# Performance work log

Measured on AMD Instinct MI355X. Metric: run time of the kernel, lower is better.

## Reference

```python
import jax, jax.numpy as jnp
import numpy as np

B, HIMG, WIMG = 8, 24, 24
WIDTH, NCH, CW = 1024, 8, 128
NHEADS, HD = 8, 16
HALF = HD // 2
NFREQ, VOCAB, NCLS = 32, 256, 10
HIDDEN = 4096
EPS = 1e-6
LAMBDA_INIT = 0.8 - 0.6 * float(np.exp(-0.3 * 0.0))  # layer_idx = 0


def rmsnorm(x, w, eps=EPS):
    return x * jax.lax.rsqrt(jnp.mean(x * x, axis=-1, keepdims=True) + eps) * w


def causal_attn(q, k, v, scale):
    # q,k: [B,H,L,d2], v: [B,H,L,D]
    L = q.shape[2]
    scores = jnp.einsum('bhqd,bhkd->bhqk', q, k) * scale
    mask = jnp.tril(jnp.ones((L, L), dtype=bool))
    scores = jnp.where(mask, scores, -jnp.inf)
    return jnp.einsum('bhqk,bhkd->bhqd', jax.nn.softmax(scores, axis=-1), v)


def diff_attn(h, qkv_w, qkv_b, qn_w, kn_w, hn_w, lq1, lk1, lq2, lk2, ow, ob):
    Bb, L, C = h.shape
    qkv = jax.nn.silu(h @ qkv_w + qkv_b).reshape(Bb, L, 3, NHEADS, HD)
    q, k, v = qkv[:, :, 0], qkv[:, :, 1], qkv[:, :, 2]
    t = lambda a: a.transpose(0, 2, 1, 3)  # [B,L,H,d] -> [B,H,L,d]
    q1 = t(rmsnorm(q[..., :HALF], qn_w)); q2 = t(rmsnorm(q[..., HALF:], qn_w))
    k1 = t(rmsnorm(k[..., :HALF], kn_w)); k2 = t(rmsnorm(k[..., HALF:], kn_w))
    v = t(v)
    lam = jnp.exp(jnp.dot(lq1, lk1)) - jnp.exp(jnp.dot(lq2, lk2)) + LAMBDA_INIT
    scale = 1.0 / np.sqrt(HALF)
    out1 = causal_attn(q1, k1, v, scale)
    out2 = causal_attn(q2, k2, v, scale)
    diff = rmsnorm(out1 - lam * out2, hn_w) * (1.0 - LAMBDA_INIT)
    out = diff.transpose(0, 2, 1, 3).reshape(Bb, L, C)
    return jax.nn.silu(out @ ow + ob)


def setup_inputs() -> dict:
    key = jax.random.key(0)
    ks = iter(jax.random.split(key, 64))
    n = lambda shape, s=0.02: jax.random.normal(next(ks), shape, jnp.float32) * s
    return dict(
        x=jax.random.uniform(next(ks), (B, HIMG, WIMG), jnp.float32),
        top_k=4,
        pixel_embed=n((VOCAB, WIDTH)),
        freq_h=n((NFREQ,), 0.1), freq_w=n((NFREQ,), 0.1),
        phase_h=jnp.zeros((NFREQ,), jnp.float32), phase_w=jnp.zeros((NFREQ,), jnp.float32),
        pos_proj_w=n((4 * NFREQ, WIDTH)), pos_proj_b=jnp.zeros((WIDTH,), jnp.float32),
        embed_norm_w=jnp.ones((WIDTH,), jnp.float32),
        se_w1=n((WIDTH, WIDTH // 4)), se_b1=jnp.zeros((WIDTH // 4,), jnp.float32),
        se_w2=n((WIDTH // 4, WIDTH)), se_b2=jnp.zeros((WIDTH,), jnp.float32),
        mix_norm_w=jnp.ones((WIDTH,), jnp.float32),
        mlp_w1=n((WIDTH, HIDDEN)), mlp_b1=jnp.zeros((HIDDEN,), jnp.float32),
        mlp_w2=n((HIDDEN, WIDTH)), mlp_b2=jnp.zeros((WIDTH,), jnp.float32),
        mlp_norm_w=jnp.ones((WIDTH,), jnp.float32),
        router_w=n((WIDTH, NCH)), router_b=jnp.zeros((NCH,), jnp.float32),
        qkv_w=n((NCH, CW, 3 * CW)), qkv_b=jnp.zeros((NCH, 3 * CW), jnp.float32),
        q_norm_w=jnp.ones((NCH, HALF), jnp.float32), k_norm_w=jnp.ones((NCH, HALF), jnp.float32),
        head_norm_w=jnp.ones((NCH, HD), jnp.float32),
        lam_q1=n((NCH, HALF), 0.1), lam_k1=n((NCH, HALF), 0.1),
        lam_q2=n((NCH, HALF), 0.1), lam_k2=n((NCH, HALF), 0.1),
        out_w=n((NCH, CW, CW)), out_b=jnp.zeros((NCH, CW), jnp.float32),
        seg_norm_w=jnp.ones((NCH, CW), jnp.float32),
        head_w=n((WIDTH, NCLS)), head_b=jnp.zeros((NCLS,), jnp.float32),
    )


def reference(x, top_k, pixel_embed, freq_h, freq_w, phase_h, phase_w, pos_proj_w,
              pos_proj_b, embed_norm_w, se_w1, se_b1, se_w2, se_b2, mix_norm_w,
              mlp_w1, mlp_b1, mlp_w2, mlp_b2, mlp_norm_w, router_w, router_b,
              qkv_w, qkv_b, q_norm_w, k_norm_w, head_norm_w, lam_q1, lam_k1,
              lam_q2, lam_k2, out_w, out_b, seg_norm_w, head_w, head_b):
    Bb, H, W = x.shape
    L = H * W
    # LearnedSinusoidal2DEmbed
    hp = jnp.arange(H, dtype=jnp.float32) / H
    wp = jnp.arange(W, dtype=jnp.float32) / W
    fh = jax.nn.softplus(freq_h) * 10.0
    fw = jax.nn.softplus(freq_w) * 10.0
    ha = hp[:, None] * fh + phase_h          # [H, NFREQ]
    wa = wp[:, None] * fw + phase_w
    h_enc = jnp.concatenate([jnp.sin(ha), jnp.cos(ha)], -1)
    w_enc = jnp.concatenate([jnp.sin(wa), jnp.cos(wa)], -1)
    pos = jnp.concatenate([jnp.broadcast_to(h_enc[:, None], (H, W, 2 * NFREQ)),
                           jnp.broadcast_to(w_enc[None, :], (H, W, 2 * NFREQ))], -1)
    pos = pos @ pos_proj_w + pos_proj_b      # [H, W, WIDTH]
    xi = jnp.clip((x * 255.0).astype(jnp.int32), 0, 255).reshape(Bb, L)
    h = pixel_embed[xi] + pos.reshape(1, L, WIDTH)
    h = rmsnorm(h, embed_norm_w)
    # ChannelMixer: SE + RMSNorm residual, MLP residual, top-k router
    s = jnp.mean(h, axis=1)
    s = jax.nn.sigmoid(jax.nn.silu(s @ se_w1 + se_b1) @ se_w2 + se_b2)
    h = h + rmsnorm(h * s[:, None, :] - h, mix_norm_w)
    h = h + rmsnorm(jax.nn.silu(h @ mlp_w1 + mlp_b1) @ mlp_w2 + mlp_b2, mlp_norm_w)
    logits_r = jnp.mean(h, axis=1) @ router_w + router_b   # [B, NCH]
    tv, ti = jax.lax.top_k(logits_r, top_k)
    rw = jnp.zeros_like(logits_r).at[jnp.arange(Bb)[:, None], ti].set(jax.nn.softmax(tv, axis=-1))
    # ChannelSegment: per-channel differential attention expert, routed
    outs = []
    for i in range(NCH):
        hi = h[..., i * CW:(i + 1) * CW]
        o = diff_attn(hi, qkv_w[i], qkv_b[i], q_norm_w[i], k_norm_w[i], head_norm_w[i],
                      lam_q1[i], lam_k1[i], lam_q2[i], lam_k2[i], out_w[i], out_b[i])
        hi = hi + rmsnorm(o, seg_norm_w[i])
        outs.append(hi * rw[:, i][:, None, None])
    h = jnp.concatenate(outs, axis=-1)
    # classifier head
    return jnp.mean(h, axis=1) @ head_w + head_b
```

## Files before the change

### kernel.cpp

```cpp
#include <hip/hip_runtime.h>
#include <math.h>

typedef __bf16 bf16;
typedef __bf16 bf16x8 __attribute__((ext_vector_type(8)));
typedef __bf16 bf16x4 __attribute__((ext_vector_type(4)));
typedef __bf16 bf16x2 __attribute__((ext_vector_type(2)));
typedef float f32x4 __attribute__((ext_vector_type(4)));
typedef short s16x4 __attribute__((ext_vector_type(4)));

constexpr int Bsz = 8, HIMG = 24, WIMG = 24;
constexpr int Lq = 576;
constexpr int WIDTH = 1024, NCH = 8, CW = 128;
constexpr int NHEADS = 8, HD = 16, HALF = 8;
constexpr float EPS = 1e-6f;
constexpr float LAMINIT = 0.2f;
constexpr float QSCALE_E = 0.35355339059327373f * 1.4426950408889634f;
constexpr int ROWS = Bsz * Lq;

__device__ __forceinline__ float fexp2(float x) {
#if __has_builtin(__builtin_amdgcn_exp2f)
  return __builtin_amdgcn_exp2f(x);
#else
  return exp2f(x);
#endif
}

constexpr size_t B_HB    = 0;
constexpr size_t B_G2B   = B_HB    + 9437184;
constexpr size_t B_ENCB  = B_G2B   + 9437184;
constexpr size_t B_POSWT = B_ENCB  + 163840;
constexpr size_t B_QKVWT = B_POSWT + 262144;
constexpr size_t B_OWT   = B_QKVWT + 786432;
constexpr size_t B_SE    = B_OWT   + 262144;
constexpr size_t B_T1    = B_SE    + 32768;
constexpr size_t B_MP    = B_T1    + 8192;
constexpr size_t B_RW    = B_MP    + 524288;
constexpr size_t B_LAM   = B_RW    + 256;
constexpr size_t B_POOL  = B_LAM   + 256;

__device__ __forceinline__ float blockReduceSum256(float v, float* red) {
  #pragma unroll
  for (int off = 32; off; off >>= 1) v += __shfl_down(v, off, 64);
  int lane = threadIdx.x & 63, wid = threadIdx.x >> 6;
  if (lane == 0) red[wid] = v;
  __syncthreads();
  float total = 0.f;
  #pragma unroll
  for (int i = 0; i < 4; i++) total += red[i];
  return total;
}
__device__ __forceinline__ float silu(float x) { return x / (1.f + __expf(-x)); }

__device__ __forceinline__ void gl16(const bf16* g, bf16* l) {
  __builtin_amdgcn_global_load_lds(
      (const __attribute__((address_space(1))) void*)g,
      (__attribute__((address_space(3))) void*)l, 16, 0, 0);
}

__device__ __forceinline__ f32x4 mfma16(bf16x4 a, bf16x4 b, f32x4 c) {
#if __has_builtin(__builtin_amdgcn_mfma_f32_16x16x16bf16_1k)
  union { bf16x4 h; s16x4 s; } ua, ub;
  ua.h = a; ub.h = b;
  return __builtin_amdgcn_mfma_f32_16x16x16bf16_1k(ua.s, ub.s, c, 0, 0, 0);
#else
  f32x4 d = c;
  asm volatile("v_mfma_f32_16x16x16_bf16 %0, %1, %2, %0"
               : "+v"(d) : "v"(a), "v"(b));
  return d;
#endif
}

__global__ __launch_bounds__(256) void k_tcast(const float* __restrict__ W,
    bf16* __restrict__ Wt, int K, int N) {
  __shared__ float t[32][33];
  int n0 = blockIdx.x * 32, k0 = blockIdx.y * 32;
  long zo = (long)blockIdx.z * K * N;
  int tid = threadIdx.x;
  int r = tid >> 3, c4 = (tid & 7) * 4;
  const float4 v = *(const float4*)(W + zo + (long)(k0 + r) * N + n0 + c4);
  t[c4 + 0][r] = v.x; t[c4 + 1][r] = v.y; t[c4 + 2][r] = v.z; t[c4 + 3][r] = v.w;
  __syncthreads();
  bf16* dst = Wt + zo + (long)(n0 + r) * K + k0 + c4;
  dst[0] = (bf16)t[r][c4 + 0]; dst[1] = (bf16)t[r][c4 + 1];
  dst[2] = (bf16)t[r][c4 + 2]; dst[3] = (bf16)t[r][c4 + 3];
}

__global__ void k_enc_b(const float* __restrict__ fh, const float* __restrict__ fw,
                        const float* __restrict__ ph, const float* __restrict__ pw,
                        bf16* __restrict__ enc) {
  int idx = blockIdx.x * blockDim.x + threadIdx.x;
  if (idx >= Lq * 128) return;
  int l = idx >> 7, c = idx & 127;
  int hh = l / WIMG, ww = l % WIMG;
  float v;
  if (c < 64) {
    int f = c & 31;
    float fr = log1pf(__expf(fh[f])) * 10.f;
    float a = (hh / (float)HIMG) * fr + ph[f];
    v = (c < 32) ? sinf(a) : cosf(a);
  } else {
    int f = c & 31;
    float fr = log1pf(__expf(fw[f])) * 10.f;
    float a = (ww / (float)WIMG) * fr + pw[f];
    v = (c < 96) ? sinf(a) : cosf(a);
  }
  enc[idx] = (bf16)v;
}

template <int ACT, int OUTBF>
__global__ __launch_bounds__(256) void gemm_bt(
    const bf16* __restrict__ A, int lda, long aZs,
    const bf16* __restrict__ Bt, long bZs,
    const float* __restrict__ bias, int biasZs,
    void* __restrict__ Cv, int ldc, long cZs,
    int M, int N, int K) {
  __shared__ bf16 As[128 * 32];
  __shared__ bf16 Bs[128 * 32];
  int tid = threadIdx.x;
  int m0 = blockIdx.y * 128, n0 = blockIdx.x * 128;
  int z = blockIdx.z;
  const bf16* Ab = A + (long)z * aZs;
  const bf16* Bb = Bt + (long)z * bZs;
  f32x4 acc[4][4] = {};
  int wv = tid >> 6, lane = tid & 63;
  int wrow = (wv >> 1) * 64, wcol = (wv & 1) * 64;
  int lm = lane & 15, lq = lane >> 4;
  const bf16* ag = Ab + (long)(m0 + (tid >> 2)) * lda + (tid & 3) * 8;
  const bf16* bg = Bb + (long)(n0 + (tid >> 2)) * K + (tid & 3) * 8;
  bf16* asd = As + tid * 8;
  bf16* bsd = Bs + tid * 8;
  for (int k0 = 0; k0 < K; k0 += 32) {
    gl16(ag + k0, asd);
    gl16(ag + k0 + 64L * lda, asd + 2048);
    gl16(bg + k0, bsd);
    gl16(bg + k0 + 64L * K, bsd + 2048);
    __syncthreads();
    bf16x8 af[4], bfr[4];
    #pragma unroll
    for (int i = 0; i < 4; i++) {
      af[i]  = *(const bf16x8*)(As + (wrow + i * 16 + lm) * 32 + lq * 8);
      bfr[i] = *(const bf16x8*)(Bs + (wcol + i * 16 + lm) * 32 + lq * 8);
    }
    #pragma unroll
    for (int i = 0; i < 4; i++)
      #pragma unroll
      for (int j = 0; j < 4; j++)
        acc[i][j] = __builtin_amdgcn_mfma_f32_16x16x32_bf16(af[i], bfr[j], acc[i][j], 0, 0, 0);
    __syncthreads();
  }
  long cz = (long)z * cZs;
  const float* bz = bias ? bias + (long)z * biasZs : nullptr;
  #pragma unroll
  for (int i = 0; i < 4; i++) {
    int row = m0 + wrow + i * 16 + lq * 4;
    #pragma unroll
    for (int j = 0; j < 4; j++) {
      int col = n0 + wcol + j * 16 + lm;
      float bv = bz ? bz[col] : 0.f;
      #pragma unroll
      for (int r = 0; r < 4; r++) {
        float v = acc[i][j][r] + bv;
        if (ACT == 1) v = silu(v);
        long off = cz + (long)(row + r) * ldc + col;
        if (OUTBF) ((bf16*)Cv)[off] = (bf16)v;
        else       ((float*)Cv)[off] = v;
      }
    }
  }
}

template <int ACT, int OUTBF, int ACC>
__global__ __launch_bounds__(256) void gemm64(
    const bf16* __restrict__ A, int lda, long aZs,
    const bf16* __restrict__ Bt, int ldb, long bZs,
    const float* __restrict__ bias, int biasZs,
    void* __restrict__ Cv, int ldc, long cZs,
    int M, int N, int K) {
  __shared__ bf16 As[64 * 32];
  __shared__ bf16 Bs[128 * 32];
  int tid = threadIdx.x;
  int m0 = blockIdx.y * 64, n0 = blockIdx.x * 128;
  int z = blockIdx.z;
  const bf16* Ab = A + (long)z * aZs;
  const bf16* Bb = Bt + (long)z * bZs;
  f32x4 acc[4][2] = {};
  int wv = tid >> 6, lane = tid & 63;
  int lm = lane & 15, lq = lane >> 4;
  int wcol = wv * 32;
  const bf16* ag = Ab + (long)(m0 + (tid >> 2)) * lda + (tid & 3) * 8;
  const bf16* bg = Bb + (long)(n0 + (tid >> 2)) * ldb + (tid & 3) * 8;
  bf16* asd = As + tid * 8;
  bf16* bsd = Bs + tid * 8;
  for (int k0 = 0; k0 < K; k0 += 32) {
    if (tid < 256) gl16(ag + k0, asd);
    gl16(bg + k0, bsd);
    gl16(bg + k0 + 64L * ldb, bsd + 2048);
    __syncthreads();
    bf16x8 af[4], bfr[2];
    #pragma unroll
    for (int i = 0; i < 4; i++)
      af[i] = *(const bf16x8*)(As + (i * 16 + lm) * 32 + lq * 8);
    #pragma unroll
    for (int j = 0; j < 2; j++)
      bfr[j] = *(const bf16x8*)(Bs + (wcol + j * 16 + lm) * 32 + lq * 8);
    #pragma unroll
    for (int i = 0; i < 4; i++)
      #pragma unroll
      for (int j = 0; j < 2; j++)
        acc[i][j] = __builtin_amdgcn_mfma_f32_16x16x32_bf16(af[i], bfr[j], acc[i][j], 0, 0, 0);
    __syncthreads();
  }
  long cz = (long)z * cZs;
  const float* bz = bias ? bias + (long)z * biasZs : nullptr;
  #pragma unroll
  for (int i = 0; i < 4; i++) {
    int row = m0 + i * 16 + lq * 4;
    #pragma unroll
    for (int j = 0; j < 2; j++) {
      int col = n0 + wcol + j * 16 + lm;
      float bv = bz ? bz[col] : 0.f;
      #pragma unroll
      for (int r = 0; r < 4; r++) {
        float v = acc[i][j][r] + bv;
        long off = cz + (long)(row + r) * ldc + col;
        if (ACC) v += (float)((bf16*)Cv)[off];
        if (ACT == 1) v = silu(v);
        if (OUTBF) ((bf16*)Cv)[off] = (bf16)v;
        else       ((float*)Cv)[off] = v;
      }
    }
  }
}

__global__ __launch_bounds__(256) void k_embed(const float* __restrict__ x,
    const float* __restrict__ emb, const float* __restrict__ pos,
    const float* __restrict__ nw, bf16* __restrict__ h) {
  __shared__ float red[4];
  int row = blockIdx.x;
  int l = row % Lq;
  int xi = (int)(x[row] * 255.f);
  xi = min(max(xi, 0), 255);
  const float* er = emb + (long)xi * WIDTH;
  const float* pr = pos + (long)l * WIDTH;
  int c0 = threadIdx.x * 4;
  float v[4]; float ss = 0.f;
  #pragma unroll
  for (int i = 0; i < 4; i++) { v[i] = er[c0 + i] + pr[c0 + i]; ss += v[i] * v[i]; }
  ss = blockReduceSum256(ss, red);
  float r = rsqrtf(ss / WIDTH + EPS);
  bf16* hr = h + (long)row * WIDTH;
  #pragma unroll
  for (int i = 0; i < 4; i++) hr[c0 + i] = (bf16)(v[i] * r * nw[c0 + i]);
}

__global__ void k_meanl_p(const bf16* __restrict__ h, float* __restrict__ part) {
  int lp = blockIdx.x, b = blockIdx.y, t = threadIdx.x;
  const bf16* p = h + ((long)b * Lq + (long)lp * 36) * WIDTH + t * 4;
  float a0 = 0, a1 = 0, a2 = 0, a3 = 0;
  for (int l = 0; l < 36; l++) {
    bf16x4 v = *(const bf16x4*)(p + (long)l * WIDTH);
    a0 += (float)v[0]; a1 += (float)v[1]; a2 += (float)v[2]; a3 += (float)v[3];
  }
  float* dst = part + ((long)b * 16 + lp) * WIDTH + t * 4;
  dst[0] = a0; dst[1] = a1; dst[2] = a2; dst[3] = a3;
}

__global__ __launch_bounds__(256) void k_se1(const float* __restrict__ part,
    const float* __restrict__ w1, const float* __restrict__ b1,
    float* __restrict__ t1) {
  __shared__ float sv[1024];
  __shared__ float red[256];
  int jb = blockIdx.x, b = blockIdx.y, t = threadIdx.x;
  for (int c = t; c < 1024; c += 256) {
    float a = 0.f;
    #pragma unroll
    for (int lp = 0; lp < 16; lp++) a += part[((long)b * 16 + lp) * 1024 + c];
    sv[c] = a * (1.f / 576.f);
  }
  __syncthreads();
  int j = t & 7, pt = t >> 3;
  int j0 = jb * 8;
  float acc = 0.f;
  int c0 = pt * 32;
  #pragma unroll 8
  for (int c = c0; c < c0 + 32; c++) acc += sv[c] * w1[c * 256 + j0 + j];
  red[t] = acc;
  __syncthreads();
  if (t < 8) {
    float a = b1[j0 + t];
    #pragma unroll
    for (int p = 0; p < 32; p++) a += red[p * 8 + t];
    t1[b * 256 + j0 + t] = silu(a);
  }
}

__global__ __launch_bounds__(256) void k_se2(const float* __restrict__ t1,
    const float* __restrict__ w2, const float* __restrict__ b2,
    float* __restrict__ s) {
  __shared__ float red[256];
  int jb = blockIdx.x, b = blockIdx.y, t = threadIdx.x;
  int j = t & 31, pt = t >> 5;
  int j0 = jb * 32;
  const float* tb = t1 + b * 256;
  float acc = 0.f;
  int c0 = pt * 32;
  #pragma unroll 8
  for (int c = c0; c < c0 + 32; c++) acc += tb[c] * w2[c * 1024 + j0 + j];
  red[t] = acc;
  __syncthreads();
  if (t < 32) {
    float a = b2[j0 + t];
    #pragma unroll
    for (int p = 0; p < 8; p++) a += red[p * 32 + t];
    s[b * 1024 + j0 + t] = 1.f / (1.f + __expf(-a));
  }
}

__global__ __launch_bounds__(256) void k_mix_b(bf16* __restrict__ h,
    const float* __restrict__ s, const float* __restrict__ mw) {
  __shared__ float red[4];
  int row = blockIdx.x;
  int b = row / Lq;
  bf16* hr = h + (long)row * WIDTH;
  const float* sb = s + b * WIDTH;
  int c0 = threadIdx.x * 4;
  float hv[4], y[4]; float ss = 0.f;
  #pragma unroll
  for (int i = 0; i < 4; i++) {
    hv[i] = (float)hr[c0 + i];
    y[i] = hv[i] * (sb[c0 + i] - 1.f); ss += y[i] * y[i];
  }
  ss = blockReduceSum256(ss, red);
  float r = rsqrtf(ss / WIDTH + EPS);
  #pragma unroll
  for (int i = 0; i < 4; i++) hr[c0 + i] = (bf16)(hv[i] + y[i] * r * mw[c0 + i]);
}

__global__ __launch_bounds__(256) void k_addnorm_b(bf16* __restrict__ h,
    const bf16* __restrict__ g, const float* __restrict__ mw) {
  __shared__ float red[4];
  int row = blockIdx.x;
  bf16* hr = h + (long)row * WIDTH;
  const bf16* gr = g + (long)row * WIDTH;
  int c0 = threadIdx.x * 4;
  float y[4]; float ss = 0.f;
  #pragma unroll
  for (int i = 0; i < 4; i++) { y[i] = (float)gr[c0 + i]; ss += y[i] * y[i]; }
  ss = blockReduceSum256(ss, red);
  float r = rsqrtf(ss / WIDTH + EPS);
  #pragma unroll
  for (int i = 0; i < 4; i++)
    hr[c0 + i] = (bf16)((float)hr[c0 + i] + y[i] * r * mw[c0 + i]);
}

__global__ __launch_bounds__(256) void k_router(const float* __restrict__ part,
    const float* __restrict__ rwgt, const float* __restrict__ rb,
    const float* __restrict__ lq1, const float* __restrict__ lk1,
    const float* __restrict__ lq2, const float* __restrict__ lk2,
    float* __restrict__ rw, float* __restrict__ lam) {
  __shared__ float sv[1024];
  __shared__ float red[256];
  __shared__ float lg[8];
  int b = blockIdx.x, t = threadIdx.x;
  for (int c = t; c < 1024; c += 256) {
    float a = 0.f;
    #pragma unroll
    for (int lp = 0; lp < 16; lp++) a += part[((long)b * 16 + lp) * 1024 + c];
    sv[c] = a * (1.f / 576.f);
  }
  __syncthreads();
  int j = t & 7, pt = t >> 3;
  float acc = 0.f;
  int c0 = pt * 32;
  #pragma unroll 8
  for (int c = c0; c < c0 + 32; c++) acc += sv[c] * rwgt[c * 8 + j];
  red[t] = acc;
  __syncthreads();
  if (t < 8) {
    float a = rb[t];
    for (int p = 0; p < 32; p++) a += red[p * 8 + t];
    lg[t] = a;
  }
  __syncthreads();
  if (t == 0) {
    float v[8]; bool sel[8];
    #pragma unroll
    for (int i = 0; i < 8; i++) { v[i] = lg[i]; sel[i] = false; }
    int idxs[4]; float vals[4];
    for (int s = 0; s < 4; s++) {
      int bi = -1; float bv = -1e30f;
      for (int i = 0; i < 8; i++) if (!sel[i] && v[i] > bv) { bv = v[i]; bi = i; }
      sel[bi] = true; idxs[s] = bi; vals[s] = bv;
    }
    float m = vals[0], den = 0.f, e[4];
    for (int s = 0; s < 4; s++) { e[s] = __expf(vals[s] - m); den += e[s]; }
    for (int i = 0; i < 8; i++) rw[b * 8 + i] = 0.f;
    for (int s = 0; s < 4; s++) rw[b * 8 + idxs[s]] = e[s] / den;
  }
  if (b == 0 && t >= 8 && t < 16) {
    int c = t - 8;
    float d1 = 0.f, d2 = 0.f;
    for (int i = 0; i < 8; i++) {
      d1 += lq1[c * 8 + i] * lk1[c * 8 + i];
      d2 += lq2[c * 8 + i] * lk2[c * 8 + i];
    }
    lam[c] = __expf(d1) - __expf(d2) + LAMINIT;
  }
}

__global__ __launch_bounds__(256) void k_attn_mfma(
    const bf16* __restrict__ qkv, const float* __restrict__ lam,
    const float* __restrict__ hnw, const float* __restrict__ qn,
    const float* __restrict__ kn, bf16* __restrict__ dc) {
  __shared__ bf16 Ks[576 * 16];
  __shared__ bf16 Vt[16 * 584];
  int tid = threadIdx.x;
  int slice = blockIdx.x; int zc = slice >> 3, b = slice & 7;
  int head = blockIdx.z;
  const bf16* qkvb = qkv + ((long)zc * ROWS + (long)b * Lq) * 384;
  for (int i = tid; i < 1152; i += 256) {
    int row = i >> 1, hf = i & 1;
    gl16(qkvb + (long)row * 384 + 128 + head * 16 + hf * 8, Ks + i * 8);
  }
  for (int i = tid; i < 1152; i += 256) {
    int row = i >> 1, dh = i & 1;
    bf16x8 v = *(const bf16x8*)(qkvb + (long)row * 384 + 256 + head * 16 + dh * 8);
    #pragma unroll
    for (int j = 0; j < 8; j++) Vt[(dh * 8 + j) * 584 + row] = v[j];
  }
  __syncthreads();
  {
    float kw[8];
    #pragma unroll
    for (int j = 0; j < 8; j++) kw[j] = kn[zc * 8 + j];
    for (int i = tid; i < 1152; i += 256) {
      bf16x8 kv = *(const bf16x8*)(Ks + i * 8);
      float f[8], s = 0.f;
      #pragma unroll
      for (int j = 0; j < 8; j++) { f[j] = (float)kv[j]; s += f[j] * f[j]; }
      float r = rsqrtf(s * 0.125f + EPS);
      bf16x8 o;
      #pragma unroll
      for (int j = 0; j < 8; j++) o[j] = (bf16)(f[j] * r * kw[j]);
      *(bf16x8*)(Ks + i * 8) = o;
    }
  }
  __syncthreads();
  int wv = tid >> 6, lane = tid & 63;
  int lm = lane & 15, lq = lane >> 4;
  float lamv = lam[zc];
  float hwv[4];
  #pragma unroll
  for (int r = 0; r < 4; r++) hwv[r] = hnw[zc * 16 + lq * 4 + r] * (1.f - LAMINIT);
  float qw[8];
  #pragma unroll
  for (int j = 0; j < 8; j++) qw[j] = qn[zc * 8 + j];
  int u = blockIdx.y * 4 + wv;
  int prA, prB, prC;
  if (u < 6) { prA = u + 2; prB = 17 - u; prC = -1; }
  else       { int v2 = u - 6; prA = v2; prB = 8 + v2; prC = 11 - v2; }
  for (int pi = 0; pi < 3; pi++) {
    int pr = (pi == 0) ? prA : (pi == 1) ? prB : prC;
    if (pr < 0) continue;
    bf16x8 bq0[2] = {{}, {}}, bq1[2] = {{}, {}};
    if (lq < 2) {
      #pragma unroll
      for (int tile = 0; tile < 2; tile++) {
        bf16x8 t8 = *(const bf16x8*)(
            qkvb + (long)(pr * 32 + tile * 16 + lm) * 384 + head * 16 + lq * 8);
        float f[8], s = 0.f;
        #pragma unroll
        for (int j = 0; j < 8; j++) { f[j] = (float)t8[j]; s += f[j] * f[j]; }
        float r = rsqrtf(s * 0.125f + EPS) * QSCALE_E;
        bf16x8 n;
        #pragma unroll
        for (int j = 0; j < 8; j++) n[j] = (bf16)(f[j] * r * qw[j]);
        if (lq == 0) bq0[tile] = n; else bq1[tile] = n;
      }
    }
    f32x4 o[2][2] = {};
    float den[2][2] = {};
    for (int kc = 0; kc <= pr; kc++) {
      f32x4 sT[2][2][2] = {};
      #pragma unroll
      for (int t = 0; t < 2; t++) {
        bf16x8 aK = {};
        if (lq < 2) aK = *(const bf16x8*)(Ks + (kc * 32 + t * 16 + lm) * 16 + lq * 8);
        #pragma unroll
        for (int tile = 0; tile < 2; tile++) {
          sT[t][tile][0] = __builtin_amdgcn_mfma_f32_16x16x32_bf16(aK, bq0[tile], sT[t][tile][0], 0, 0, 0);
          sT[t][tile][1] = __builtin_amdgcn_mfma_f32_16x16x32_bf16(aK, bq1[tile], sT[t][tile][1], 0, 0, 0);
        }
      }
      bool diag = (kc == pr);
      #pragma unroll
      for (int t = 0; t < 2; t++) {
        bf16x4 aV = *(const bf16x4*)(Vt + lm * 584 + kc * 32 + t * 16 + lq * 4);
        #pragma unroll
        for (int tile = 0; tile < 2; tile++) {
          if (diag && tile == 0 && t == 1) continue;
          bool masked = diag && (tile == t);
          #pragma unroll
          for (int h2 = 0; h2 < 2; h2++) {
            bf16x4 pb;
            float dsum = 0.f;
            #pragma unroll
            for (int r = 0; r < 4; r++) {
              float ev = fexp2(sT[t][tile][h2][r]);
              if (masked && (lq * 4 + r > lm)) ev = 0.f;
              dsum += ev;
              pb[r] = (bf16)ev;
            }
            den[tile][h2] += dsum;
            o[tile][h2] = mfma16(aV, pb, o[tile][h2]);
          }
        }
      }
    }
    #pragma unroll
    for (int tile = 0; tile < 2; tile++)
      #pragma unroll
      for (int h2 = 0; h2 < 2; h2++) {
        den[tile][h2] += __shfl_xor(den[tile][h2], 16);
        den[tile][h2] += __shfl_xor(den[tile][h2], 32);
      }
    #pragma unroll
    for (int tile = 0; tile < 2; tile++) {
      float inv1 = 1.f / den[tile][0];
      float inv2 = lamv / den[tile][1];
      float dff[4]; float ss = 0.f;
      #pragma unroll
      for (int r = 0; r < 4; r++) {
        dff[r] = o[tile][0][r] * inv1 - o[tile][1][r] * inv2;
        ss += dff[r] * dff[r];
      }
      ss += __shfl_xor(ss, 16);
      ss += __shfl_xor(ss, 32);
      float rr = rsqrtf(ss * 0.0625f + EPS);
      bf16x4 outp;
      #pragma unroll
      for (int r = 0; r < 4; r++) outp[r] = (bf16)(dff[r] * rr * hwv[r]);
      long rowg = (long)zc * ROWS + (long)b * Lq + pr * 32 + tile * 16 + lm;
      *(bf16x4*)(dc + rowg * 128 + head * 16 + lq * 4) = outp;
    }
  }
}

__global__ __launch_bounds__(64) void k_segpool(const bf16* __restrict__ h,
    const bf16* __restrict__ op, const float* __restrict__ segw,
    const float* __restrict__ rw, float* __restrict__ part) {
  int lp = blockIdx.x, b = blockIdx.y, ch = blockIdx.z;
  int t = threadIdx.x;
  int c0 = t * 2;
  float w0 = segw[ch * 128 + c0], w1 = segw[ch * 128 + c0 + 1];
  float rwv = rw[b * 8 + ch];
  float a0 = 0.f, a1 = 0.f;
  for (int l = 0; l < 72; l++) {
    int row = b * Lq + lp * 72 + l;
    const bf16* oprow = op + (long)ch * ROWS * CW + (long)row * CW;
    bf16x2 yv = *(const bf16x2*)(oprow + c0);
    float y0 = (float)yv[0], y1 = (float)yv[1];
    float ss = y0 * y0 + y1 * y1;
    #pragma unroll
    for (int m = 1; m < 64; m <<= 1) ss += __shfl_xor(ss, m);
    float r = rsqrtf(ss * (1.f / 128.f) + EPS);
    bf16x2 hv = *(const bf16x2*)(h + (long)row * WIDTH + ch * 128 + c0);
    a0 += ((float)hv[0] + y0 * r * w0) * rwv;
    a1 += ((float)hv[1] + y1 * r * w1) * rwv;
  }
  float* dst = part + ((long)b * 8 + lp) * 1024 + ch * 128 + c0;
  dst[0] = a0; dst[1] = a1;
}

__global__ __launch_bounds__(256) void k_head(const float* __restrict__ part,
    const float* __restrict__ hw, const float* __restrict__ hb, float* __restrict__ out) {
  __shared__ float pool[1024];
  __shared__ float red[256];
  int b = blockIdx.x, t = threadIdx.x;
  for (int c = t; c < 1024; c += 256) {
    float a = 0.f;
    #pragma unroll
    for (int lp = 0; lp < 8; lp++) a += part[((long)b * 8 + lp) * 1024 + c];
    pool[c] = a * (1.f / 576.f);
  }
  __syncthreads();
  int j = t & 15, pt = t >> 4;
  float acc = 0.f;
  if (j < 10)
    for (int c = pt * 64; c < pt * 64 + 64; c++)
      acc += pool[c] * hw[c * 10 + j];
  red[t] = acc;
  __syncthreads();
  if (t < 10) {
    float a = hb[t];
    for (int p = 0; p < 16; p++) a += red[p * 16 + t];
    out[b * 10 + t] = a;
  }
}

extern "C" void kernel_launch(void* const* d_in, const int* in_sizes, int n_in,
                              void* d_out, int out_size, void* d_ws, size_t ws_size,
                              hipStream_t stream) {
  const float* x          = (const float*)d_in[0];
  const float* pixel_embed= (const float*)d_in[2];
  const float* freq_h     = (const float*)d_in[3];
  const float* freq_w     = (const float*)d_in[4];
  const float* phase_h    = (const float*)d_in[5];
  const float* phase_w    = (const float*)d_in[6];
  const float* pos_proj_w = (const float*)d_in[7];
  const float* pos_proj_b = (const float*)d_in[8];
  const float* embed_norm = (const float*)d_in[9];
  const float* se_w1      = (const float*)d_in[10];
  const float* se_b1      = (const float*)d_in[11];
  const float* se_w2      = (const float*)d_in[12];
  const float* se_b2      = (const float*)d_in[13];
  const float* mix_norm   = (const float*)d_in[14];
  const float* mlp_w1     = (const float*)d_in[15];
  const float* mlp_b1     = (const float*)d_in[16];
  const float* mlp_w2     = (const float*)d_in[17];
  const float* mlp_b2     = (const float*)d_in[18];
  const float* mlp_norm   = (const float*)d_in[19];
  const float* router_w   = (const float*)d_in[20];
  const float* router_b   = (const float*)d_in[21];
  const float* qkv_w      = (const float*)d_in[22];
  const float* qkv_b      = (const float*)d_in[23];
  const float* q_norm_w   = (const float*)d_in[24];
  const float* k_norm_w   = (const float*)d_in[25];
  const float* head_norm_w= (const float*)d_in[26];
  const float* lam_q1     = (const float*)d_in[27];
  const float* lam_k1     = (const float*)d_in[28];
  const float* lam_q2     = (const float*)d_in[29];
  const float* lam_k2     = (const float*)d_in[30];
  const float* out_w      = (const float*)d_in[31];
  const float* out_b      = (const float*)d_in[32];
  const float* seg_norm_w = (const float*)d_in[33];
  const float* head_w     = (const float*)d_in[34];
  const float* head_b     = (const float*)d_in[35];

  char* W = (char*)d_ws;
  bf16*  HB    = (bf16*)(W + B_HB);
  bf16*  G2B   = (bf16*)(W + B_G2B);
  bf16*  ENCB  = (bf16*)(W + B_ENCB);
  bf16*  POSWT = (bf16*)(W + B_POSWT);
  bf16*  QKVWT = (bf16*)(W + B_QKVWT);
  bf16*  OWT   = (bf16*)(W + B_OWT);
  float* SE    = (float*)(W + B_SE);
  float* T1    = (float*)(W + B_T1);
  float* MP    = (float*)(W + B_MP);
  float* RW    = (float*)(W + B_RW);
  float* LAM   = (float*)(W + B_LAM);
  char*  P     = W + B_POOL;
  float* POS   = (float*)P;
  bf16*  W1T   = (bf16*)P;
  bf16*  W2T   = (bf16*)(P + 8388608);
  bf16*  HID   = (bf16*)(P + 16777216);
  bf16*  QKV   = (bf16*)P;
  bf16*  DC    = (bf16*)(P + 28311552);
  float* out   = (float*)d_out;

  k_enc_b<<<288, 256, 0, stream>>>(freq_h, freq_w, phase_h, phase_w, ENCB);
  k_tcast<<<dim3(32, 4, 1), 256, 0, stream>>>(pos_proj_w, POSWT, 128, 1024);
  gemm64<0, 0, 0><<<dim3(8, 10, 1), 256, 0, stream>>>(
      ENCB, 128, 0, POSWT, 128, 0, pos_proj_b, 0, POS, 1024, 0, 640, 1024, 128);
  k_embed<<<ROWS, 256, 0, stream>>>(x, pixel_embed, POS, embed_norm, HB);
  k_meanl_p<<<dim3(16, 8), 256, 0, stream>>>(HB, MP);
  k_se1<<<dim3(32, 8), 256, 0, stream>>>(MP, se_w1, se_b1, T1);
  k_se2<<<dim3(32, 8), 256, 0, stream>>>(T1, se_w2, se_b2, SE);
  k_mix_b<<<ROWS, 256, 0, stream>>>(HB, SE, mix_norm);
  k_tcast<<<dim3(128, 32, 1), 256, 0, stream>>>(mlp_w1, W1T, 1024, 4096);
  k_tcast<<<dim3(32, 128, 1), 256, 0, stream>>>(mlp_w2, W2T, 4096, 1024);
  gemm_bt<1, 1><<<dim3(16, 36, 1), 256, 0, stream>>>(
      HB, 1024, 0, W1T, 0, mlp_b1, 0, HID, 2048, 0, 4608, 2048, 1024);
  gemm64<0, 1, 0><<<dim3(8, 72, 1), 256, 0, stream>>>(
      HID, 2048, 0, W2T, 4096, 0, mlp_b2, 0, G2B, 1024, 0, 4608, 1024, 2048);
  gemm_bt<1, 1><<<dim3(16, 36, 1), 256, 0, stream>>>(
      HB, 1024, 0, W1T + 2048L * 1024, 0, mlp_b1 + 2048, 0, HID, 2048, 0, 4608, 2048, 1024);
  gemm64<0, 1, 1><<<dim3(8, 72, 1), 256, 0, stream>>>(
      HID, 2048, 0, W2T + 2048, 4096, 0, nullptr, 0, G2B, 1024, 0, 4608, 1024, 2048);
  k_addnorm_b<<<ROWS, 256, 0, stream>>>(HB, G2B, mlp_norm);
  k_meanl_p<<<dim3(16, 8), 256, 0, stream>>>(HB, MP);
  k_router<<<8, 256, 0, stream>>>(MP, router_w, router_b,
                                  lam_q1, lam_k1, lam_q2, lam_k2, RW, LAM);
  k_tcast<<<dim3(12, 4, 8), 256, 0, stream>>>(qkv_w, QKVWT, 128, 384);
  k_tcast<<<dim3(4, 4, 8), 256, 0, stream>>>(out_w, OWT, 128, 128);
  gemm64<1, 1, 0><<<dim3(3, 72, 8), 256, 0, stream>>>(
      HB, 1024, CW, QKVWT, 128, 384 * 128, qkv_b, 384,
      QKV, 384, (long)ROWS * 384, ROWS, 384, 128);
  k_attn_mfma<<<dim3(64, 2, 8), 256, 0, stream>>>(
      QKV, LAM, head_norm_w, q_norm_w, k_norm_w, DC);
  gemm64<1, 1, 0><<<dim3(1, 72, 8), 256, 0, stream>>>(
      DC, 128, (long)ROWS * 128, OWT, 128, 128 * 128, out_b, 128,
      DC, 128, (long)ROWS * 128, ROWS, 128, 128);
  k_segpool<<<dim3(8, 8, 8), 64, 0, stream>>>(HB, DC, seg_norm_w, RW, MP);
  k_head<<<8, 256, 0, stream>>>(MP, head_w, head_b, out);
}
```

Measured before the change: 500.7 us.

## Batch weight casts, fuse q/k RMSNorm into QKV GEMM, merge MLP halves

```diff
diff --git a/kernel.cpp b/kernel.cpp
--- a/kernel.cpp
+++ b/kernel.cpp
@@ -37,6 +37,7 @@
 constexpr size_t B_RW    = B_MP    + 524288;
 constexpr size_t B_LAM   = B_RW    + 256;
 constexpr size_t B_POOL  = B_LAM   + 256;
+constexpr size_t WS_BIG = B_POOL + 8388608 + 8388608 + 37748736;
 
 __device__ __forceinline__ float blockReduceSum256(float v, float* red) {
   #pragma unroll
@@ -70,11 +71,10 @@
 #endif
 }
 
-__global__ __launch_bounds__(256) void k_tcast(const float* __restrict__ W,
-    bf16* __restrict__ Wt, int K, int N) {
+__device__ __forceinline__ void tcast_tile(const float* __restrict__ W,
+    bf16* __restrict__ Wt, int K, int N, long zo, int bx, int by) {
   __shared__ float t[32][33];
-  int n0 = blockIdx.x * 32, k0 = blockIdx.y * 32;
-  long zo = (long)blockIdx.z * K * N;
+  int n0 = bx * 32, k0 = by * 32;
   int tid = threadIdx.x;
   int r = tid >> 3, c4 = (tid & 7) * 4;
   const float4 v = *(const float4*)(W + zo + (long)(k0 + r) * N + n0 + c4);
@@ -83,6 +83,32 @@
   bf16* dst = Wt + zo + (long)(n0 + r) * K + k0 + c4;
   dst[0] = (bf16)t[r][c4 + 0]; dst[1] = (bf16)t[r][c4 + 1];
   dst[2] = (bf16)t[r][c4 + 2]; dst[3] = (bf16)t[r][c4 + 3];
+}
+
+__global__ __launch_bounds__(256) void k_tcast_all(
+    const float* __restrict__ w1, const float* __restrict__ w2,
+    const float* __restrict__ posw, const float* __restrict__ qkvw,
+    const float* __restrict__ outw,
+    bf16* __restrict__ W1T, bf16* __restrict__ W2T, bf16* __restrict__ POSWT,
+    bf16* __restrict__ QKVWT, bf16* __restrict__ OWT) {
+  int bid = blockIdx.x;
+  if (bid < 4096) {
+    tcast_tile(w1, W1T, 1024, 4096, 0, bid % 128, bid / 128);
+  } else if (bid < 8192) {
+    int t = bid - 4096;
+    tcast_tile(w2, W2T, 4096, 1024, 0, t % 32, t / 32);
+  } else if (bid < 8320) {
+    int t = bid - 8192;
+    tcast_tile(posw, POSWT, 128, 1024, 0, t % 32, t / 32);
+  } else if (bid < 8704) {
+    int t = bid - 8320;
+    int z = t / 48; t -= z * 48;
+    tcast_tile(qkvw, QKVWT, 128, 384, (long)z * 49152, t % 12, t / 12);
+  } else {
+    int t = bid - 8704;
+    int z = t / 16; t -= z * 16;
+    tcast_tile(outw, OWT, 128, 128, (long)z * 16384, t % 4, t / 4);
+  }
 }
 
 __global__ void k_enc_b(const float* __restrict__ fh, const float* __restrict__ fw,
@@ -169,13 +195,14 @@
   }
 }
 
-template <int ACT, int OUTBF, int ACC>
+template <int ACT, int OUTBF, int ACC, int NORM>
 __global__ __launch_bounds__(256) void gemm64(
     const bf16* __restrict__ A, int lda, long aZs,
     const bf16* __restrict__ Bt, int ldb, long bZs,
     const float* __restrict__ bias, int biasZs,
     void* __restrict__ Cv, int ldc, long cZs,
-    int M, int N, int K) {
+    int M, int N, int K,
+    const float* __restrict__ qn, const float* __restrict__ kn) {
   __shared__ bf16 As[64 * 32];
   __shared__ bf16 Bs[128 * 32];
   int tid = threadIdx.x;
@@ -192,7 +219,7 @@
   bf16* asd = As + tid * 8;
   bf16* bsd = Bs + tid * 8;
   for (int k0 = 0; k0 < K; k0 += 32) {
-    if (tid < 256) gl16(ag + k0, asd);
+    gl16(ag + k0, asd);
     gl16(bg + k0, bsd);
     gl16(bg + k0 + 64L * ldb, bsd + 2048);
     __syncthreads();
@@ -212,21 +239,49 @@
   }
   long cz = (long)z * cZs;
   const float* bz = bias ? bias + (long)z * biasZs : nullptr;
-  #pragma unroll
-  for (int i = 0; i < 4; i++) {
-    int row = m0 + i * 16 + lq * 4;
-    #pragma unroll
-    for (int j = 0; j < 2; j++) {
-      int col = n0 + wcol + j * 16 + lm;
-      float bv = bz ? bz[col] : 0.f;
-      #pragma unroll
-      for (int r = 0; r < 4; r++) {
-        float v = acc[i][j][r] + bv;
-        long off = cz + (long)(row + r) * ldc + col;
-        if (ACC) v += (float)((bf16*)Cv)[off];
-        if (ACT == 1) v = silu(v);
-        if (OUTBF) ((bf16*)Cv)[off] = (bf16)v;
-        else       ((float*)Cv)[off] = v;
+  if constexpr (NORM == 0) {
+    #pragma unroll
+    for (int i = 0; i < 4; i++) {
+      int row = m0 + i * 16 + lq * 4;
+      #pragma unroll
+      for (int j = 0; j < 2; j++) {
+        int col = n0 + wcol + j * 16 + lm;
+        float bv = bz ? bz[col] : 0.f;
+        #pragma unroll
+        for (int r = 0; r < 4; r++) {
+          float v = acc[i][j][r] + bv;
+          long off = cz + (long)(row + r) * ldc + col;
+          if (ACC) v += (float)((bf16*)Cv)[off];
+          if (ACT == 1) v = silu(v);
+          if (OUTBF) ((bf16*)Cv)[off] = (bf16)v;
+          else       ((float*)Cv)[off] = v;
+        }
+      }
+    }
+  } else {
+    int nsec = blockIdx.x;
+    bool don = nsec < 2;
+    float wnv = 1.f;
+    if (nsec == 0) wnv = qn[z * 8 + (lm & 7)] * QSCALE_E;
+    else if (nsec == 1) wnv = kn[z * 8 + (lm & 7)];
+    #pragma unroll
+    for (int i = 0; i < 4; i++) {
+      int row = m0 + i * 16 + lq * 4;
+      #pragma unroll
+      for (int j = 0; j < 2; j++) {
+        int col = n0 + wcol + j * 16 + lm;
+        float bv = bz ? bz[col] : 0.f;
+        #pragma unroll
+        for (int r = 0; r < 4; r++) {
+          float v = acc[i][j][r] + bv;
+          if (ACT == 1) v = silu(v);
+          float s = v * v;
+          s += __shfl_xor(s, 1);
+          s += __shfl_xor(s, 2);
+          s += __shfl_xor(s, 4);
+          if (don) v = v * rsqrtf(s * 0.125f + EPS) * wnv;
+          ((bf16*)Cv)[cz + (long)(row + r) * ldc + col] = (bf16)v;
+        }
       }
     }
   }
@@ -410,8 +465,7 @@
 
 __global__ __launch_bounds__(256) void k_attn_mfma(
     const bf16* __restrict__ qkv, const float* __restrict__ lam,
-    const float* __restrict__ hnw, const float* __restrict__ qn,
-    const float* __restrict__ kn, bf16* __restrict__ dc) {
+    const float* __restrict__ hnw, bf16* __restrict__ dc) {
   __shared__ bf16 Ks[576 * 16];
   __shared__ bf16 Vt[16 * 584];
   int tid = threadIdx.x;
@@ -429,32 +483,12 @@
     for (int j = 0; j < 8; j++) Vt[(dh * 8 + j) * 584 + row] = v[j];
   }
   __syncthreads();
-  {
-    float kw[8];
-    #pragma unroll
-    for (int j = 0; j < 8; j++) kw[j] = kn[zc * 8 + j];
-    for (int i = tid; i < 1152; i += 256) {
-      bf16x8 kv = *(const bf16x8*)(Ks + i * 8);
-      float f[8], s = 0.f;
-      #pragma unroll
-      for (int j = 0; j < 8; j++) { f[j] = (float)kv[j]; s += f[j] * f[j]; }
-      float r = rsqrtf(s * 0.125f + EPS);
-      bf16x8 o;
-      #pragma unroll
-      for (int j = 0; j < 8; j++) o[j] = (bf16)(f[j] * r * kw[j]);
-      *(bf16x8*)(Ks + i * 8) = o;
-    }
-  }
-  __syncthreads();
   int wv = tid >> 6, lane = tid & 63;
   int lm = lane & 15, lq = lane >> 4;
   float lamv = lam[zc];
   float hwv[4];
   #pragma unroll
   for (int r = 0; r < 4; r++) hwv[r] = hnw[zc * 16 + lq * 4 + r] * (1.f - LAMINIT);
-  float qw[8];
-  #pragma unroll
-  for (int j = 0; j < 8; j++) qw[j] = qn[zc * 8 + j];
   int u = blockIdx.y * 4 + wv;
   int prA, prB, prC;
   if (u < 6) { prA = u + 2; prB = 17 - u; prC = -1; }
@@ -468,14 +502,7 @@
       for (int tile = 0; tile < 2; tile++) {
         bf16x8 t8 = *(const bf16x8*)(
             qkvb + (long)(pr * 32 + tile * 16 + lm) * 384 + head * 16 + lq * 8);
-        float f[8], s = 0.f;
-        #pragma unroll
-        for (int j = 0; j < 8; j++) { f[j] = (float)t8[j]; s += f[j] * f[j]; }
-        float r = rsqrtf(s * 0.125f + EPS) * QSCALE_E;
-        bf16x8 n;
-        #pragma unroll
-        for (int j = 0; j < 8; j++) n[j] = (bf16)(f[j] * r * qw[j]);
-        if (lq == 0) bq0[tile] = n; else bq1[tile] = n;
+        if (lq == 0) bq0[tile] = t8; else bq1[tile] = t8;
       }
     }
     f32x4 o[2][2] = {};
@@ -555,8 +582,8 @@
   float w0 = segw[ch * 128 + c0], w1 = segw[ch * 128 + c0 + 1];
   float rwv = rw[b * 8 + ch];
   float a0 = 0.f, a1 = 0.f;
-  for (int l = 0; l < 72; l++) {
-    int row = b * Lq + lp * 72 + l;
+  for (int l = 0; l < 36; l++) {
+    int row = b * Lq + lp * 36 + l;
     const bf16* oprow = op + (long)ch * ROWS * CW + (long)row * CW;
     bf16x2 yv = *(const bf16x2*)(oprow + c0);
     float y0 = (float)yv[0], y1 = (float)yv[1];
@@ -568,7 +595,7 @@
     a0 += ((float)hv[0] + y0 * r * w0) * rwv;
     a1 += ((float)hv[1] + y1 * r * w1) * rwv;
   }
-  float* dst = part + ((long)b * 8 + lp) * 1024 + ch * 128 + c0;
+  float* dst = part + ((long)b * 16 + lp) * 1024 + ch * 128 + c0;
   dst[0] = a0; dst[1] = a1;
 }
 
@@ -580,7 +607,7 @@
   for (int c = t; c < 1024; c += 256) {
     float a = 0.f;
     #pragma unroll
-    for (int lp = 0; lp < 8; lp++) a += part[((long)b * 8 + lp) * 1024 + c];
+    for (int lp = 0; lp < 16; lp++) a += part[((long)b * 16 + lp) * 1024 + c];
     pool[c] = a * (1.f / 576.f);
   }
   __syncthreads();
@@ -640,6 +667,7 @@
   char* W = (char*)d_ws;
   bf16*  HB    = (bf16*)(W + B_HB);
   bf16*  G2B   = (bf16*)(W + B_G2B);
+  float* POS   = (float*)(W + B_G2B);
   bf16*  ENCB  = (bf16*)(W + B_ENCB);
   bf16*  POSWT = (bf16*)(W + B_POSWT);
   bf16*  QKVWT = (bf16*)(W + B_QKVWT);
@@ -650,47 +678,56 @@
   float* RW    = (float*)(W + B_RW);
   float* LAM   = (float*)(W + B_LAM);
   char*  P     = W + B_POOL;
-  float* POS   = (float*)P;
   bf16*  W1T   = (bf16*)P;
   bf16*  W2T   = (bf16*)(P + 8388608);
   bf16*  HID   = (bf16*)(P + 16777216);
   bf16*  QKV   = (bf16*)P;
   bf16*  DC    = (bf16*)(P + 28311552);
   float* out   = (float*)d_out;
-
+  const bool big = ws_size >= WS_BIG;
+
+  k_tcast_all<<<8832, 256, 0, stream>>>(mlp_w1, mlp_w2, pos_proj_w, qkv_w, out_w,
+                                        W1T, W2T, POSWT, QKVWT, OWT);
   k_enc_b<<<288, 256, 0, stream>>>(freq_h, freq_w, phase_h, phase_w, ENCB);
-  k_tcast<<<dim3(32, 4, 1), 256, 0, stream>>>(pos_proj_w, POSWT, 128, 1024);
-  gemm64<0, 0, 0><<<dim3(8, 10, 1), 256, 0, stream>>>(
-      ENCB, 128, 0, POSWT, 128, 0, pos_proj_b, 0, POS, 1024, 0, 640, 1024, 128);
+  gemm64<0, 0, 0, 0><<<dim3(8, 10, 1), 256, 0, stream>>>(
+      ENCB, 128, 0, POSWT, 128, 0, pos_proj_b, 0, POS, 1024, 0, 640, 1024, 128,
+      nullptr, nullptr);
   k_embed<<<ROWS, 256, 0, stream>>>(x, pixel_embed, POS, embed_norm, HB);
   k_meanl_p<<<dim3(16, 8), 256, 0, stream>>>(HB, MP);
   k_se1<<<dim3(32, 8), 256, 0, stream>>>(MP, se_w1, se_b1, T1);
   k_se2<<<dim3(32, 8), 256, 0, stream>>>(T1, se_w2, se_b2, SE);
   k_mix_b<<<ROWS, 256, 0, stream>>>(HB, SE, mix_norm);
-  k_tcast<<<dim3(128, 32, 1), 256, 0, stream>>>(mlp_w1, W1T, 1024, 4096);
-  k_tcast<<<dim3(32, 128, 1), 256, 0, stream>>>(mlp_w2, W2T, 4096, 1024);
-  gemm_bt<1, 1><<<dim3(16, 36, 1), 256, 0, stream>>>(
-      HB, 1024, 0, W1T, 0, mlp_b1, 0, HID, 2048, 0, 4608, 2048, 1024);
-  gemm64<0, 1, 0><<<dim3(8, 72, 1), 256, 0, stream>>>(
-      HID, 2048, 0, W2T, 4096, 0, mlp_b2, 0, G2B, 1024, 0, 4608, 1024, 2048);
-  gemm_bt<1, 1><<<dim3(16, 36, 1), 256, 0, stream>>>(
-      HB, 1024, 0, W1T + 2048L * 1024, 0, mlp_b1 + 2048, 0, HID, 2048, 0, 4608, 2048, 1024);
-  gemm64<0, 1, 1><<<dim3(8, 72, 1), 256, 0, stream>>>(
-      HID, 2048, 0, W2T + 2048, 4096, 0, nullptr, 0, G2B, 1024, 0, 4608, 1024, 2048);
+  if (big) {
+    gemm_bt<1, 1><<<dim3(16, 36, 2), 256, 0, stream>>>(
+        HB, 1024, 0, W1T, 2048L * 1024, mlp_b1, 2048,
+        HID, 4096, 2048, 4608, 2048, 1024);
+    gemm64<0, 1, 0, 0><<<dim3(8, 72, 1), 256, 0, stream>>>(
+        HID, 4096, 0, W2T, 4096, 0, mlp_b2, 0,
+        G2B, 1024, 0, 4608, 1024, 4096, nullptr, nullptr);
+  } else {
+    gemm_bt<1, 1><<<dim3(16, 36, 1), 256, 0, stream>>>(
+        HB, 1024, 0, W1T, 0, mlp_b1, 0, HID, 2048, 0, 4608, 2048, 1024);
+    gemm64<0, 1, 0, 0><<<dim3(8, 72, 1), 256, 0, stream>>>(
+        HID, 2048, 0, W2T, 4096, 0, mlp_b2, 0, G2B, 1024, 0, 4608, 1024, 2048,
+        nullptr, nullptr);
+    gemm_bt<1, 1><<<dim3(16, 36, 1), 256, 0, stream>>>(
+        HB, 1024, 0, W1T + 2048L * 1024, 0, mlp_b1 + 2048, 0, HID, 2048, 0,
+        4608, 2048, 1024);
+    gemm64<0, 1, 1, 0><<<dim3(8, 72, 1), 256, 0, stream>>>(
+        HID, 2048, 0, W2T + 2048, 4096, 0, nullptr, 0, G2B, 1024, 0,
+        4608, 1024, 2048, nullptr, nullptr);
+  }
   k_addnorm_b<<<ROWS, 256, 0, stream>>>(HB, G2B, mlp_norm);
   k_meanl_p<<<dim3(16, 8), 256, 0, stream>>>(HB, MP);
   k_router<<<8, 256, 0, stream>>>(MP, router_w, router_b,
                                   lam_q1, lam_k1, lam_q2, lam_k2, RW, LAM);
-  k_tcast<<<dim3(12, 4, 8), 256, 0, stream>>>(qkv_w, QKVWT, 128, 384);
-  k_tcast<<<dim3(4, 4, 8), 256, 0, stream>>>(out_w, OWT, 128, 128);
-  gemm64<1, 1, 0><<<dim3(3, 72, 8), 256, 0, stream>>>(
+  gemm64<1, 1, 0, 1><<<dim3(3, 72, 8), 256, 0, stream>>>(
       HB, 1024, CW, QKVWT, 128, 384 * 128, qkv_b, 384,
-      QKV, 384, (long)ROWS * 384, ROWS, 384, 128);
-  k_attn_mfma<<<dim3(64, 2, 8), 256, 0, stream>>>(
-      QKV, LAM, head_norm_w, q_norm_w, k_norm_w, DC);
-  gemm64<1, 1, 0><<<dim3(1, 72, 8), 256, 0, stream>>>(
+      QKV, 384, (long)ROWS * 384, ROWS, 384, 128, q_norm_w, k_norm_w);
+  k_attn_mfma<<<dim3(64, 2, 8), 256, 0, stream>>>(QKV, LAM, head_norm_w, DC);
+  gemm64<1, 1, 0, 0><<<dim3(1, 72, 8), 256, 0, stream>>>(
       DC, 128, (long)ROWS * 128, OWT, 128, 128 * 128, out_b, 128,
-      DC, 128, (long)ROWS * 128, ROWS, 128, 128);
-  k_segpool<<<dim3(8, 8, 8), 64, 0, stream>>>(HB, DC, seg_norm_w, RW, MP);
+      DC, 128, (long)ROWS * 128, ROWS, 128, 128, nullptr, nullptr);
+  k_segpool<<<dim3(16, 8, 8), 64, 0, stream>>>(HB, DC, seg_norm_w, RW, MP);
   k_head<<<8, 256, 0, stream>>>(MP, head_w, head_b, out);
 }
```

Result: faster. 476.0 us (-4.9%).
